# Kernel optimization log

Measured on AMD Instinct MI355X. Metric: run time of the kernel, lower is better.

## Reference

```python
import jax, jax.numpy as jnp
import numpy as np


def setup_inputs() -> dict:
    key = jax.random.key(0)
    k1, k2, k3, k4, k5 = jax.random.split(key, 5)
    d_in, d_out, r = 1024, 1024, 32
    x = jax.random.normal(k1, (8, 8192, d_in), dtype=jnp.float32)
    W = jax.random.normal(k2, (d_out, d_in), dtype=jnp.float32) * (1.0 / np.sqrt(d_in))
    b = jax.random.normal(k3, (d_out,), dtype=jnp.float32) * 0.01
    V_r = jax.random.normal(k4, (d_in, r), dtype=jnp.float32) * (1.0 / np.sqrt(d_in))
    C = jax.random.normal(k5, (d_out, r), dtype=jnp.float32) * (1.0 / np.sqrt(r))
    return {"x": x, "W": W, "b": b, "V_r": V_r, "C": C}


def reference(x, W, b, V_r, C):
    # base = x @ W.T + b  (the quantized linear, modeled in fp32)
    base = jnp.einsum('bsd,od->bso', x, W) + b
    # low-rank correction: (x @ V_r) @ C.T  -- keep factored form, never
    # materialize the dense d_in x d_out correction matrix
    correction = jnp.einsum('bsr,or->bso', jnp.einsum('bsd,dr->bsr', x, V_r), C)
    return base + correction
```

## Files before the change

### kernel.cpp

```cpp
#include <hip/hip_runtime.h>
#include <hip/hip_bf16.h>

typedef __bf16 bf16_t;
typedef __bf16 bf16x8 __attribute__((ext_vector_type(8)));
typedef float  f32x4  __attribute__((ext_vector_type(4)));

#define DK 1024
#define DN 1024
#define RNK 32
#define BM 128
#define BN 512
#define BK 32
#define NKT 32

__global__ void weff_kernel(const float* __restrict__ W,
                            const float* __restrict__ Vr,
                            const float* __restrict__ C,
                            bf16_t* __restrict__ WeffSw)
{
    const int o  = blockIdx.x;
    const int g  = threadIdx.x;
    const int d0 = g * 8;

    f32x4 cv[8];
#pragma unroll
    for (int q = 0; q < 8; ++q) cv[q] = *(const f32x4*)(C + o * RNK + q * 4);

    const f32x4* wrow = (const f32x4*)(W + (size_t)o * DK + d0);
    f32x4 w0 = wrow[0], w1 = wrow[1];
    float acc[8];
#pragma unroll
    for (int e = 0; e < 4; ++e) { acc[e] = w0[e]; acc[4 + e] = w1[e]; }

#pragma unroll
    for (int e = 0; e < 8; ++e) {
        const f32x4* vre = (const f32x4*)(Vr + (size_t)(d0 + e) * RNK);
        float s = 0.f;
#pragma unroll
        for (int q = 0; q < 8; ++q) {
            f32x4 v = vre[q];
            s += cv[q][0] * v[0] + cv[q][1] * v[1] + cv[q][2] * v[2] + cv[q][3] * v[3];
        }
        acc[e] += s;
    }

    bf16x8 out;
#pragma unroll
    for (int e = 0; e < 8; ++e) out[e] = (bf16_t)acc[e];

    const int bn = o >> 9, rloc = o & 511;
    const int kt = d0 >> 5, seg = (d0 >> 3) & 3;
    const int sw = seg ^ ((rloc >> 1) & 3);
    const size_t byte = (size_t)(bn * 32 + kt) * 32768 + rloc * 64 + (sw << 4);
    *(bf16x8*)((char*)WeffSw + byte) = out;
}

__global__ __launch_bounds__(512, 1) void corrlin_gemm_kernel(
    const float* __restrict__ X, const bf16_t* __restrict__ WeffSw,
    const float* __restrict__ bias, float* __restrict__ Out)
{
    __shared__ __align__(16) char smem[81920];
    char* Ab0 = smem;
    char* Ab1 = smem + 8192;
    char* Bb0 = smem + 16384;
    char* Bb1 = smem + 49152;

    const int tid = threadIdx.x;
    const int b0  = blockIdx.x;
    const int L  = (b0 & 7) * 128 + (b0 >> 3);
    const int bm = L >> 1;
    const int bn = L & 1;
    const int m0 = bm * BM;

    const int lane = tid & 63;
    const int wn   = tid >> 6;
    const int arow = tid >> 2;
    const int aseg = tid & 3;

    f32x4 acc[8][4] = {};
    f32x4 set0[2], set1[2];

    auto issueA = [&](int kt, f32x4* s) {
        const float* p = X + (size_t)(m0 + arow) * DK + kt * BK + aseg * 8;
        s[0] = *(const f32x4*)p;
        s[1] = *(const f32x4*)(p + 4);
    };
    auto storeA = [&](const f32x4* s, char* Ab) {
        const int sw = aseg ^ ((arow >> 1) & 3);
        bf16x8 v;
#pragma unroll
        for (int j = 0; j < 4; ++j) { v[j] = (bf16_t)s[0][j]; v[4 + j] = (bf16_t)s[1][j]; }
        *(bf16x8*)(Ab + arow * 64 + (sw << 4)) = v;
    };
    auto issueB = [&](int kt, char* Bb) {
        const char* g = (const char*)WeffSw + (size_t)(bn * 32 + kt) * 32768;
#pragma unroll
        for (int c = 0; c < 4; ++c) {
            const int lin = c * 8192 + wn * 1024;
            __builtin_amdgcn_global_load_lds(
                (const __attribute__((address_space(1))) void*)(g + lin + lane * 16),
                (__attribute__((address_space(3))) void*)(Bb + lin),
                16, 0, 0);
        }
    };
    auto readB = [&](const char* Bc, bf16x8* bfr) {
        const int kb = lane >> 4;
#pragma unroll
        for (int nf = 0; nf < 4; ++nf) {
            const int row = wn * 64 + nf * 16 + (lane & 15);
            bfr[nf] = *(const bf16x8*)(Bc + row * 64 + ((kb ^ ((row >> 1) & 3)) << 4));
        }
    };
    auto compute_h = [&](const char* Ac, int h, const bf16x8* bfr) {
        bf16x8 af[4];
        const int kb = lane >> 4;
#pragma unroll
        for (int i = 0; i < 4; ++i) {
            const int row = (h * 4 + i) * 16 + (lane & 15);
            af[i] = *(const bf16x8*)(Ac + row * 64 + ((kb ^ ((row >> 1) & 3)) << 4));
        }
        __builtin_amdgcn_s_setprio(1);
#pragma unroll
        for (int i = 0; i < 4; ++i)
#pragma unroll
            for (int nf = 0; nf < 4; ++nf)
                acc[h * 4 + i][nf] = __builtin_amdgcn_mfma_f32_16x16x32_bf16(
                    af[i], bfr[nf], acc[h * 4 + i][nf], 0, 0, 0);
        __builtin_amdgcn_s_setprio(0);
    };

    auto iter = [&](int t, const char* Ac, const char* Bc, char* An, char* Bn,
                    f32x4* aStore , f32x4* aFill ) {
        if (t + 1 < NKT) issueB(t + 1, Bn);
        bf16x8 bfr[4];
        readB(Bc, bfr);
        compute_h(Ac, 0, bfr);
        if (t + 1 < NKT) storeA(aStore, An);
        if (t + 2 < NKT) issueA(t + 2, aFill);
        compute_h(Ac, 1, bfr);
        if (t + 2 < NKT) {
            asm volatile("s_waitcnt vmcnt(2) lgkmcnt(0)" ::: "memory");
            __builtin_amdgcn_s_barrier();
        } else if (t + 1 < NKT) {
            asm volatile("s_waitcnt vmcnt(0) lgkmcnt(0)" ::: "memory");
            __builtin_amdgcn_s_barrier();
        }
    };

    issueA(0, set0);
    issueB(0, Bb0);
    storeA(set0, Ab0);
    issueA(1, set1);
    asm volatile("s_waitcnt vmcnt(2) lgkmcnt(0)" ::: "memory");
    __builtin_amdgcn_s_barrier();

    for (int t = 0; t < NKT; t += 2) {
        iter(t,     Ab0, Bb0, Ab1, Bb1, set1, set0);
        iter(t + 1, Ab1, Bb1, Ab0, Bb0, set0, set1);
    }
    __syncthreads();

    float* tb = (float*)smem + wn * 1280;
    const int nbase = bn * BN + wn * 64;
    float bv[4];
#pragma unroll
    for (int nf = 0; nf < 4; ++nf) bv[nf] = bias[nbase + nf * 16 + (lane & 15)];

#pragma unroll
    for (int mf = 0; mf < 8; ++mf) {
#pragma unroll
        for (int nf = 0; nf < 4; ++nf)
#pragma unroll
            for (int j = 0; j < 4; ++j) {
                const int r = (lane >> 4) * 4 + j;
                const int c = nf * 16 + (lane & 15);
                tb[r * 80 + c] = acc[mf][nf][j] + bv[nf];
            }
        __syncthreads();
#pragma unroll
        for (int jj = 0; jj < 4; ++jj) {
            const int rr = jj * 4 + (lane >> 4);
            const int cc = (lane & 15) * 4;
            f32x4 v = *(const f32x4*)&tb[rr * 80 + cc];
            *(f32x4*)&Out[(size_t)(m0 + mf * 16 + rr) * DN + nbase + cc] = v;
        }
        __syncthreads();
    }
}

extern "C" void kernel_launch(void* const* d_in, const int* in_sizes, int n_in,
                              void* d_out, int out_size, void* d_ws, size_t ws_size,
                              hipStream_t stream) {
    const float* x  = (const float*)d_in[0];
    const float* W  = (const float*)d_in[1];
    const float* b  = (const float*)d_in[2];
    const float* Vr = (const float*)d_in[3];
    const float* C  = (const float*)d_in[4];
    float* out = (float*)d_out;

    const int M = in_sizes[0] / DK;
    bf16_t* WeffSw = (bf16_t*)d_ws;

    weff_kernel<<<DN, 128, 0, stream>>>(W, Vr, C, WeffSw);

    const int mtiles = M / BM;
    const int nwg = mtiles * (DN / BN);
    corrlin_gemm_kernel<<<nwg, 512, 0, stream>>>(x, WeffSw, b, out);
}
```

Measured before the change: 204.3 us.

## Stream fp32 A tiles via direct global-to-LDS DMA with triple-buffered staging

A-tile loads from X now go straight from global memory into LDS using global_load_lds into a three-deep fp32 staging ring with an XOR swizzle, instead of passing through registers. A separate conversion step turns each staged fp32 tile into swizzled bf16 in LDS one stage ahead of the MFMA work. The aim is to free VGPRs and take global-load latency for the fp32 activations off the critical path. In exchange the kernel uses 128KB of LDS, does an extra LDS read/write per element for the conversion, and relies on tuned vmcnt wait counts.

```diff
diff --git a/kernel.cpp b/kernel.cpp
--- a/kernel.cpp
+++ b/kernel.cpp
@@ -55,15 +55,18 @@
     *(bf16x8*)((char*)WeffSw + byte) = out;
 }
 
-__global__ __launch_bounds__(512, 1) void corrlin_gemm_kernel(
+__global__ __launch_bounds__(512, 1) void corrlin_gemm_dma(
     const float* __restrict__ X, const bf16_t* __restrict__ WeffSw,
     const float* __restrict__ bias, float* __restrict__ Out)
 {
-    __shared__ __align__(16) char smem[81920];
-    char* Ab0 = smem;
-    char* Ab1 = smem + 8192;
-    char* Bb0 = smem + 16384;
-    char* Bb1 = smem + 49152;
+    __shared__ __align__(16) char smem[131072];
+    char* Af0 = smem;
+    char* Af1 = smem + 16384;
+    char* Af2 = smem + 32768;
+    char* Ab0 = smem + 49152;
+    char* Ab1 = smem + 57344;
+    char* Bq0 = smem + 65536;
+    char* Bq1 = smem + 98304;
 
     const int tid = threadIdx.x;
     const int b0  = blockIdx.x;
@@ -74,23 +77,21 @@
 
     const int lane = tid & 63;
     const int wn   = tid >> 6;
-    const int arow = tid >> 2;
-    const int aseg = tid & 3;
 
     f32x4 acc[8][4] = {};
-    f32x4 set0[2], set1[2];
-
-    auto issueA = [&](int kt, f32x4* s) {
-        const float* p = X + (size_t)(m0 + arow) * DK + kt * BK + aseg * 8;
-        s[0] = *(const f32x4*)p;
-        s[1] = *(const f32x4*)(p + 4);
-    };
-    auto storeA = [&](const f32x4* s, char* Ab) {
-        const int sw = aseg ^ ((arow >> 1) & 3);
-        bf16x8 v;
-#pragma unroll
-        for (int j = 0; j < 4; ++j) { v[j] = (bf16_t)s[0][j]; v[4 + j] = (bf16_t)s[1][j]; }
-        *(bf16x8*)(Ab + arow * 64 + (sw << 4)) = v;
+
+    auto issueA = [&](int kt, char* Af) {
+#pragma unroll
+        for (int c = 0; c < 2; ++c) {
+            const int d   = wn * 128 + c * 64 + lane;
+            const int row = d >> 3;
+            const int g   = (d & 7) ^ (row & 7);
+            const float* src = X + (size_t)(m0 + row) * DK + kt * 32 + g * 4;
+            __builtin_amdgcn_global_load_lds(
+                (const __attribute__((address_space(1))) void*)src,
+                (__attribute__((address_space(3))) void*)(Af + wn * 2048 + c * 1024),
+                16, 0, 0);
+        }
     };
     auto issueB = [&](int kt, char* Bb) {
         const char* g = (const char*)WeffSw + (size_t)(bn * 32 + kt) * 32768;
@@ -103,6 +104,17 @@
                 16, 0, 0);
         }
     };
+    auto convertA = [&](const char* Af, char* Abb) {
+        const int row = tid >> 2;
+        const int qs  = tid & 3;
+        const int r7  = row & 7;
+        f32x4 v0 = *(const f32x4*)(Af + row * 128 + (((2 * qs)     ^ r7) << 4));
+        f32x4 v1 = *(const f32x4*)(Af + row * 128 + (((2 * qs + 1) ^ r7) << 4));
+        bf16x8 v;
+#pragma unroll
+        for (int j = 0; j < 4; ++j) { v[j] = (bf16_t)v0[j]; v[4 + j] = (bf16_t)v1[j]; }
+        *(bf16x8*)(Abb + row * 64 + ((qs ^ ((row >> 1) & 3)) << 4)) = v;
+    };
     auto readB = [&](const char* Bc, bf16x8* bfr) {
         const int kb = lane >> 4;
 #pragma unroll
@@ -111,13 +123,13 @@
             bfr[nf] = *(const bf16x8*)(Bc + row * 64 + ((kb ^ ((row >> 1) & 3)) << 4));
         }
     };
-    auto compute_h = [&](const char* Ac, int h, const bf16x8* bfr) {
+    auto compute_h = [&](const char* Abb, int h, const bf16x8* bfr) {
         bf16x8 af[4];
         const int kb = lane >> 4;
 #pragma unroll
         for (int i = 0; i < 4; ++i) {
             const int row = (h * 4 + i) * 16 + (lane & 15);
-            af[i] = *(const bf16x8*)(Ac + row * 64 + ((kb ^ ((row >> 1) & 3)) << 4));
+            af[i] = *(const bf16x8*)(Abb + row * 64 + ((kb ^ ((row >> 1) & 3)) << 4));
         }
         __builtin_amdgcn_s_setprio(1);
 #pragma unroll
@@ -129,35 +141,59 @@
         __builtin_amdgcn_s_setprio(0);
     };
 
-    auto iter = [&](int t, const char* Ac, const char* Bc, char* An, char* Bn,
-                    f32x4* aStore , f32x4* aFill ) {
-        if (t + 1 < NKT) issueB(t + 1, Bn);
+    auto iterM = [&](int t, const char* Bc, char* Bn, const char* Abt,
+                     const char* AfN, char* AbN, char* AfI) {
+        issueB(t + 1, Bn);
+        issueA(t + 3, AfI);
+        convertA(AfN, AbN);
         bf16x8 bfr[4];
         readB(Bc, bfr);
-        compute_h(Ac, 0, bfr);
-        if (t + 1 < NKT) storeA(aStore, An);
-        if (t + 2 < NKT) issueA(t + 2, aFill);
-        compute_h(Ac, 1, bfr);
-        if (t + 2 < NKT) {
-            asm volatile("s_waitcnt vmcnt(2) lgkmcnt(0)" ::: "memory");
-            __builtin_amdgcn_s_barrier();
-        } else if (t + 1 < NKT) {
+        compute_h(Abt, 0, bfr);
+        compute_h(Abt, 1, bfr);
+        asm volatile("s_waitcnt vmcnt(2) lgkmcnt(0)" ::: "memory");
+        __builtin_amdgcn_s_barrier();
+    };
+    auto iterT = [&](int t, const char* Bc, char* Bn, const char* Abt,
+                     const char* AfN, char* AbN, char* AfI) {
+        if (t + 1 < NKT) issueB(t + 1, Bn);
+        if (t + 3 < NKT) issueA(t + 3, AfI);
+        if (t + 1 < NKT) convertA(AfN, AbN);
+        bf16x8 bfr[4];
+        readB(Bc, bfr);
+        compute_h(Abt, 0, bfr);
+        compute_h(Abt, 1, bfr);
+        if (t + 1 < NKT) {
             asm volatile("s_waitcnt vmcnt(0) lgkmcnt(0)" ::: "memory");
             __builtin_amdgcn_s_barrier();
         }
     };
 
-    issueA(0, set0);
-    issueB(0, Bb0);
-    storeA(set0, Ab0);
-    issueA(1, set1);
+    issueB(0, Bq0);
+    issueA(0, Af0);
+    issueA(1, Af1);
+    issueA(2, Af2);
+    asm volatile("s_waitcnt vmcnt(4)" ::: "memory");
+    __builtin_amdgcn_s_barrier();
+    convertA(Af0, Ab0);
     asm volatile("s_waitcnt vmcnt(2) lgkmcnt(0)" ::: "memory");
     __builtin_amdgcn_s_barrier();
 
-    for (int t = 0; t < NKT; t += 2) {
-        iter(t,     Ab0, Bb0, Ab1, Bb1, set1, set0);
-        iter(t + 1, Ab1, Bb1, Ab0, Bb0, set0, set1);
+    for (int t = 0; t < 24; t += 6) {
+        iterM(t,     Bq0, Bq1, Ab0, Af1, Ab1, Af0);
+        iterM(t + 1, Bq1, Bq0, Ab1, Af2, Ab0, Af1);
+        iterM(t + 2, Bq0, Bq1, Ab0, Af0, Ab1, Af2);
+        iterM(t + 3, Bq1, Bq0, Ab1, Af1, Ab0, Af0);
+        iterM(t + 4, Bq0, Bq1, Ab0, Af2, Ab1, Af1);
+        iterM(t + 5, Bq1, Bq0, Ab1, Af0, Ab0, Af2);
     }
+    iterT(24, Bq0, Bq1, Ab0, Af1, Ab1, Af0);
+    iterT(25, Bq1, Bq0, Ab1, Af2, Ab0, Af1);
+    iterT(26, Bq0, Bq1, Ab0, Af0, Ab1, Af2);
+    iterT(27, Bq1, Bq0, Ab1, Af1, Ab0, Af0);
+    iterT(28, Bq0, Bq1, Ab0, Af2, Ab1, Af1);
+    iterT(29, Bq1, Bq0, Ab1, Af0, Ab0, Af2);
+    iterT(30, Bq0, Bq1, Ab0, Af1, Ab1, Af0);
+    iterT(31, Bq1, Bq0, Ab1, Af2, Ab0, Af1);
     __syncthreads();
 
     float* tb = (float*)smem + wn * 1280;
@@ -205,5 +241,5 @@
 
     const int mtiles = M / BM;
     const int nwg = mtiles * (DN / BN);
-    corrlin_gemm_kernel<<<nwg, 512, 0, stream>>>(x, WeffSw, b, out);
+    corrlin_gemm_dma<<<nwg, 512, 0, stream>>>(x, WeffSw, b, out);
 }
```

Result: no change. 204.7 us (+0.2%).
